# Kernel tuning notes

Hardware: AMD Instinct MI355X
Metric: run time of the kernel (lower is better)

The kernel has to match this reference:

```python
import jax, jax.numpy as jnp
import numpy as np

H = 4      # num_heads
D = 256    # hidden_dim
HD = 64    # head_dim
SCALE = HD ** -0.5


def setup_inputs() -> dict:
    key = jax.random.key(0)
    ks = jax.random.split(key, 5)
    x = jax.random.normal(ks[0], (4, 4096, D), dtype=jnp.float32)
    # Linear weights stored torch-style as [out, in]; y = x @ W.T
    init = 1.0 / np.sqrt(D)
    Wq = jax.random.uniform(ks[1], (D, D), jnp.float32, -init, init)
    Wk = jax.random.uniform(ks[2], (D, D), jnp.float32, -init, init)
    Wv = jax.random.uniform(ks[3], (D, D), jnp.float32, -init, init)
    Wo = jax.random.uniform(ks[4], (D, D), jnp.float32, -init, init)
    return {"x": x, "Wq": Wq, "Wk": Wk, "Wv": Wv, "Wo": Wo}


def reference(x, Wq, Wk, Wv, Wo):
    B, S, _ = x.shape
    # projections (torch Linear: x @ W.T)
    q = (x @ Wq.T).reshape(B, S, H, HD).transpose(0, 2, 1, 3)  # [B,H,S,HD]
    k = (x @ Wk.T).reshape(B, S, H, HD).transpose(0, 2, 1, 3)
    v = (x @ Wv.T).reshape(B, S, H, HD).transpose(0, 2, 1, 3)
    scores = jnp.einsum('bhqd,bhkd->bhqk', q, k) * SCALE  # [B,H,S,S]
    causal = jnp.triu(jnp.ones((S, S), dtype=bool), k=1)
    scores = jnp.where(causal[None, None], -jnp.inf, scores)
    attn = jax.nn.softmax(scores, axis=-1)
    out = jnp.einsum('bhqk,bhkd->bhqd', attn, v)  # [B,H,S,HD]
    out = out.transpose(0, 2, 1, 3).reshape(B, S, D)
    return out @ Wo.T
```

## Files before the change

kernel.cpp:

```cpp
#include <hip/hip_runtime.h>
#include <hip/hip_bf16.h>
#include <cstdint>

using short8  = __attribute__((ext_vector_type(8))) short;
using u16x8   = __attribute__((ext_vector_type(8))) unsigned short;
using u16x4   = __attribute__((ext_vector_type(4))) unsigned short;
using f32x4   = __attribute__((ext_vector_type(4))) float;
using f32x16  = __attribute__((ext_vector_type(16))) float;

constexpr int BN = 4, HN = 4, SN = 4096, DN = 256, HD = 64;
constexpr int MROWS = BN * SN;
constexpr float QSCL = 0.18033688011112042f;

__device__ __forceinline__ unsigned short f2bf(float x) {
  union { float f; unsigned int u; } c; c.f = x;
  unsigned int u = c.u;
  return (unsigned short)((u + 0x7fffu + ((u >> 16) & 1u)) >> 16);
}
__device__ __forceinline__ unsigned int cvt_pk_bf16(float a, float b) {
  unsigned int r;
  asm("v_cvt_pk_bf16_f32 %0, %1, %2" : "=v"(r) : "v"(a), "v"(b));
  return r;
}
__device__ __forceinline__ void pl32swap(unsigned int& a, unsigned int& b) {
  asm volatile("v_permlane32_swap_b32 %0, %1" : "+v"(a), "+v"(b));
}

#define GLDS16(g, l)                                                  \
  __builtin_amdgcn_global_load_lds(                                   \
      (const __attribute__((address_space(1))) void*)(g),             \
      (__attribute__((address_space(3))) void*)(l), 16, 0, 0)

__global__ __launch_bounds__(256) void convert_kernel(
    const float* __restrict__ x,  const float* __restrict__ Wq,
    const float* __restrict__ Wk, const float* __restrict__ Wv,
    const float* __restrict__ Wo,
    unsigned short* __restrict__ xb, unsigned short* __restrict__ Wcat,
    unsigned short* __restrict__ Wob) {
  const long NX4 = (long)MROWS * DN / 4;
  const long NW4 = 65536 / 4;
  const long total = NX4 + 4 * NW4;
  for (long i = (long)blockIdx.x * 256 + threadIdx.x; i < total;
       i += (long)gridDim.x * 256) {
    const float* src; unsigned short* dst;
    if (i < NX4) { src = x + i * 4; dst = xb + i * 4; }
    else {
      long j = i - NX4; int w = (int)(j >> 14); long o = (j & 16383) * 4;
      src = (w == 0 ? Wq : w == 1 ? Wk : w == 2 ? Wv : Wo) + o;
      dst = (w < 3 ? Wcat + (long)w * 65536 : Wob) + o;
    }
    float4 v = *(const float4*)src;
    u16x4 pk; pk[0] = f2bf(v.x); pk[1] = f2bf(v.y);
    pk[2] = f2bf(v.z); pk[3] = f2bf(v.w);
    *(u16x4*)dst = pk;
  }
}

template <int MODE, int NBN>
__global__ __launch_bounds__(256) void gemm_kernel(
    const unsigned short* __restrict__ Abf,
    const unsigned short* __restrict__ Bbf,
    unsigned short* __restrict__ qo, unsigned short* __restrict__ ko,
    unsigned short* __restrict__ vo, float* __restrict__ out) {
  constexpr int SMEM = (MODE == 1) ? 128 * 132 * 4 : 128 * 136 * 2;
  __shared__ __align__(16) char smem[SMEM];
  unsigned short* stg = (unsigned short*)smem;

  const int tid = threadIdx.x, lane = tid & 63, wid = tid >> 6;
  const int lo = lane & 15, hi = lane >> 4;
  const int bn = blockIdx.x % NBN, bm = blockIdx.x / NBN;
  const int wm = (wid >> 1) * 64, wn = (wid & 1) * 64;
  const long arow0 = (long)bm * 128, brow0 = (long)bn * 128;

  auto stage = [&](int buf, int kt) {
    const int row = (wid * 2) * 16 + (lane >> 2);
    const int col = (lane & 3) * 8;
    const unsigned short* ga = Abf + (arow0 + row) * DN + kt * 32 + col;
    const unsigned short* gb = Bbf + (brow0 + row) * DN + kt * 32 + col;
    unsigned short* la = stg + buf * 8192 + wid * 1024;
    unsigned short* lb = la + 4096;
    GLDS16(ga, la);
    GLDS16(ga + 16 * DN, la + 512);
    GLDS16(gb, lb);
    GLDS16(gb + 16 * DN, lb + 512);
  };

  f32x4 acc[4][4];
#pragma unroll
  for (int a = 0; a < 4; ++a)
#pragma unroll
    for (int b = 0; b < 4; ++b)
#pragma unroll
      for (int e = 0; e < 4; ++e) acc[a][b][e] = 0.f;

  stage(0, 0);
#pragma unroll
  for (int kt = 0; kt < 8; ++kt) {
    const int buf = kt & 1;
    __syncthreads();
    if (kt < 7) stage(buf ^ 1, kt + 1);
    const unsigned short* sa = stg + buf * 8192;
    const unsigned short* sb = sa + 4096;
    short8 af[4], bf[4];
#pragma unroll
    for (int f = 0; f < 4; ++f) {
      af[f] = *(const short8*)(sa + (wm + f * 16 + lo) * 32 + hi * 8);
      bf[f] = *(const short8*)(sb + (wn + f * 16 + lo) * 32 + hi * 8);
    }
#pragma unroll
    for (int fn = 0; fn < 4; ++fn)
#pragma unroll
      for (int fm = 0; fm < 4; ++fm)
        acc[fn][fm] = __builtin_amdgcn_mfma_f32_16x16x32_bf16(
            bf[fn], af[fm], acc[fn][fm], 0, 0, 0);
  }
  __syncthreads();

  if constexpr (MODE == 0) {
    unsigned short* cs = (unsigned short*)smem;
    if (bn < 4) {
      const float cscl = (bn < 2) ? QSCL : 1.0f;
#pragma unroll
      for (int fn = 0; fn < 4; ++fn)
#pragma unroll
        for (int fm = 0; fm < 4; ++fm) {
          u16x4 pk;
#pragma unroll
          for (int r = 0; r < 4; ++r) pk[r] = f2bf(acc[fn][fm][r] * cscl);
          const int m = wm + fm * 16 + lo, n0 = wn + fn * 16 + hi * 4;
          *(u16x4*)(cs + m * 136 + n0) = pk;
        }
      __syncthreads();
      unsigned short* dstmat = (bn < 2) ? qo : ko;
      const int colbase = (bn & 1) * 128;
#pragma unroll
      for (int p = 0; p < 8; ++p) {
        const int ml = p * 16 + (tid >> 4), n0 = (tid & 15) * 8;
        u16x8 v = *(u16x8*)(cs + ml * 136 + n0);
        const int c = colbase + n0, h = c >> 6, hd = c & 63;
        const long m = arow0 + ml;
        const int b = (int)(m >> 12), s = (int)(m & 4095);
        *(u16x8*)(dstmat + ((long)(b * HN + h) * SN + s) * HD + hd) = v;
      }
    } else {
#pragma unroll
      for (int fn = 0; fn < 4; ++fn)
#pragma unroll
        for (int fm = 0; fm < 4; ++fm) {
          const int m = wm + fm * 16 + lo, n0 = wn + fn * 16 + hi * 4;
#pragma unroll
          for (int r = 0; r < 4; ++r)
            cs[(n0 + r) * 136 + m] = f2bf(acc[fn][fm][r]);
        }
      __syncthreads();
      const int b = (int)(arow0 >> 12), sbase = (int)(arow0 & 4095);
#pragma unroll
      for (int p = 0; p < 8; ++p) {
        const int cl = p * 16 + (tid >> 4);
        const int s0 = (tid & 15) * 8;
        u16x8 v = *(u16x8*)(cs + cl * 136 + s0);
        const int c = (bn & 1) * 128 + cl, h = c >> 6, hd = c & 63;
        *(u16x8*)(vo + ((long)((b * HN + h) * HD + hd)) * SN + sbase + s0) = v;
      }
    }
  } else {
    float* csf = (float*)smem;
#pragma unroll
    for (int fn = 0; fn < 4; ++fn)
#pragma unroll
      for (int fm = 0; fm < 4; ++fm) {
        const int m = wm + fm * 16 + lo, n0 = wn + fn * 16 + hi * 4;
        *(f32x4*)(csf + m * 132 + n0) = acc[fn][fm];
      }
    __syncthreads();
#pragma unroll
    for (int p = 0; p < 8; ++p) {
      const int ml = p * 16 + (tid >> 4), n0 = (tid & 15) * 8;
      f32x4 v0 = *(f32x4*)(csf + ml * 132 + n0);
      f32x4 v1 = *(f32x4*)(csf + ml * 132 + n0 + 4);
      float* dst = out + (arow0 + ml) * DN + bn * 128 + n0;
      *(f32x4*)dst = v0;
      *(f32x4*)(dst + 4) = v1;
    }
  }
}

template <int NSPLIT>
__global__ __launch_bounds__(256, 2) void attn_kernel(
    const unsigned short* __restrict__ Qw, const unsigned short* __restrict__ Kw,
    const unsigned short* __restrict__ VTp, unsigned short* __restrict__ Ow,
    float* __restrict__ Op, float* __restrict__ Mp, float* __restrict__ Lp) {
  __shared__ __align__(16) unsigned short sK[2][4096];
  __shared__ __align__(16) unsigned short sV[2][4096];

  const int tid = threadIdx.x;
  const int w = tid >> 6, lane = tid & 63;
  const int l31 = lane & 31, h5 = lane >> 5;
  const int bid = blockIdx.x;
  const int bh = (bid & 7) * 2 + ((bid >> 3) & 1);
  int c, g;
  if constexpr (NSPLIT == 2) { c = (bid >> 4) & 1; g = bid >> 5; }
  else { c = 0; g = bid >> 4; }
  const int t = 31 - g;
  const int q0 = t * 128;
  const int qw = q0 + w * 32;
  const long base = (long)bh * SN * HD;
  const int tlast = 2 * t + 1;
  const int wlast = 2 * t + (w >> 1);

  const int sr = w * 16 + (lane >> 3);
  const int gcol8 = (((lane & 7) ^ (lane >> 3)) << 3);
  auto stage = [&](int buf, int k0) {
    const unsigned short* gk = Kw + base + (long)(k0 + sr) * HD + gcol8;
    GLDS16(gk, &sK[buf][w * 1024]);
    GLDS16(gk + 8 * HD, &sK[buf][w * 1024 + 512]);
    const unsigned short* gv = VTp + base + (long)sr * SN + k0 + gcol8;
    GLDS16(gv, &sV[buf][w * 1024]);
    GLDS16(gv + 8 * SN, &sV[buf][w * 1024 + 512]);
  };

  short8 qf[4];
#pragma unroll
  for (int ks = 0; ks < 4; ++ks)
    qf[ks] = *(const short8*)(Qw + base + (long)(qw + l31) * HD + ks * 16 + h5 * 8);

  f32x16 oacc[2];
#pragma unroll
  for (int oh = 0; oh < 2; ++oh)
#pragma unroll
    for (int r = 0; r < 16; ++r) oacc[oh][r] = 0.f;
  float m_ = -INFINITY, l_ = 0.f;

  const int swz = (l31 & 7) << 3;

  stage(0, c * 64);
  __syncthreads();
  int buf = 0;
  for (int kt = c; kt <= tlast; kt += NSPLIT) {
    if (kt + NSPLIT <= tlast) stage(buf ^ 1, (kt + NSPLIT) * 64);

    if (kt <= wlast) {
      const int k0 = kt * 64;
      short8 kb[8];
#pragma unroll
      for (int s = 0; s < 2; ++s)
#pragma unroll
        for (int ks = 0; ks < 4; ++ks)
          kb[s * 4 + ks] = *(const short8*)&sK[buf][(32 * s + l31) * 64 +
                                                   (((2 * ks + h5) << 3) ^ swz)];
      f32x16 c0, c1;
#pragma unroll
      for (int r = 0; r < 16; ++r) { c0[r] = 0.f; c1[r] = 0.f; }
#pragma unroll
      for (int ks = 0; ks < 4; ++ks)
        c0 = __builtin_amdgcn_mfma_f32_32x32x16_bf16(kb[ks], qf[ks], c0, 0, 0, 0);
#pragma unroll
      for (int ks = 0; ks < 4; ++ks)
        c1 = __builtin_amdgcn_mfma_f32_32x32x16_bf16(kb[4 + ks], qf[ks], c1, 0, 0, 0);

      short8 vt0[4], vt1[4];
#pragma unroll
      for (int ks = 0; ks < 4; ++ks) {
        const int col = ((2 * ks + h5) << 3) ^ swz;
        vt0[ks] = *(const short8*)&sV[buf][l31 * 64 + col];
        vt1[ks] = *(const short8*)&sV[buf][(32 + l31) * 64 + col];
      }

      if (kt == wlast) {
        const int mb0 = k0 + 4 * h5 - qw - l31;
#pragma unroll
        for (int r = 0; r < 16; ++r) {
          const int d = (r & 3) + 8 * (r >> 2);
          if (mb0 + d > 0)      c0[r] = -INFINITY;
          if (mb0 + 32 + d > 0) c1[r] = -INFINITY;
        }
      }

      float mv[16];
#pragma unroll
      for (int r = 0; r < 16; ++r) mv[r] = fmaxf(c0[r], c1[r]);
#pragma unroll
      for (int st = 8; st >= 1; st >>= 1)
#pragma unroll
        for (int i = 0; i < st; ++i) mv[i] = fmaxf(mv[i], mv[i + st]);
      const float mx = fmaxf(mv[0], __shfl_xor(mv[0], 32, 64));

      if (__any(mx > m_ + 11.5f)) {
        const float mn = fmaxf(m_, mx);
        const float alpha = __builtin_amdgcn_exp2f(m_ - mn);
        m_ = mn;
        l_ *= alpha;
#pragma unroll
        for (int oh = 0; oh < 2; ++oh)
#pragma unroll
          for (int r = 0; r < 16; ++r) oacc[oh][r] *= alpha;
      }

#pragma unroll
      for (int r = 0; r < 16; ++r) {
        c0[r] = __builtin_amdgcn_exp2f(c0[r] - m_);
        c1[r] = __builtin_amdgcn_exp2f(c1[r] - m_);
      }
      float sv[16];
#pragma unroll
      for (int r = 0; r < 16; ++r) sv[r] = c0[r] + c1[r];
#pragma unroll
      for (int st = 8; st >= 1; st >>= 1)
#pragma unroll
        for (int i = 0; i < st; ++i) sv[i] += sv[i + st];
      l_ += sv[0] + __shfl_xor(sv[0], 32, 64);

      short8 pb[4];
#pragma unroll
      for (int s = 0; s < 2; ++s)
#pragma unroll
        for (int u = 0; u < 2; ++u) {
          unsigned int a0, a1, b0, b1;
          if (s == 0) {
            a0 = cvt_pk_bf16(c0[8 * u + 0], c0[8 * u + 1]);
            a1 = cvt_pk_bf16(c0[8 * u + 2], c0[8 * u + 3]);
            b0 = cvt_pk_bf16(c0[8 * u + 4], c0[8 * u + 5]);
            b1 = cvt_pk_bf16(c0[8 * u + 6], c0[8 * u + 7]);
          } else {
            a0 = cvt_pk_bf16(c1[8 * u + 0], c1[8 * u + 1]);
            a1 = cvt_pk_bf16(c1[8 * u + 2], c1[8 * u + 3]);
            b0 = cvt_pk_bf16(c1[8 * u + 4], c1[8 * u + 5]);
            b1 = cvt_pk_bf16(c1[8 * u + 6], c1[8 * u + 7]);
          }
          pl32swap(a0, b0);
          pl32swap(a1, b1);
          union { unsigned int u4[4]; short8 v; } pu;
          pu.u4[0] = a0; pu.u4[1] = a1; pu.u4[2] = b0; pu.u4[3] = b1;
          pb[s * 2 + u] = pu.v;
        }

#pragma unroll
      for (int ks = 0; ks < 4; ++ks) {
        oacc[0] = __builtin_amdgcn_mfma_f32_32x32x16_bf16(vt0[ks], pb[ks], oacc[0], 0, 0, 0);
        oacc[1] = __builtin_amdgcn_mfma_f32_32x32x16_bf16(vt1[ks], pb[ks], oacc[1], 0, 0, 0);
      }
    }

    __syncthreads();
    buf ^= 1;
  }

  if constexpr (NSPLIT == 1) {
    unsigned short* ob = (unsigned short*)sK;
    const float rl = 1.f / l_;
#pragma unroll
    for (int oh = 0; oh < 2; ++oh)
#pragma unroll
      for (int rq = 0; rq < 4; ++rq) {
        const int hdb = 32 * oh + 8 * rq + 4 * h5;
        const unsigned int u0 = cvt_pk_bf16(oacc[oh][4 * rq + 0] * rl,
                                            oacc[oh][4 * rq + 1] * rl);
        const unsigned int u1 = cvt_pk_bf16(oacc[oh][4 * rq + 2] * rl,
                                            oacc[oh][4 * rq + 3] * rl);
        *(uint2*)&ob[w * 2048 + l31 * 64 + (hdb ^ ((l31 & 7) << 3))] =
            make_uint2(u0, u1);
      }
    __syncthreads();
    const int b = bh >> 2, h = bh & 3;
#pragma unroll
    for (int pass = 0; pass < 4; ++pass) {
      const int idx = pass * 256 + tid;
      const int row = idx >> 3, j = idx & 7;
      const int wreg = row >> 5, qi = row & 31;
      u16x8 vv = *(u16x8*)&ob[wreg * 2048 + qi * 64 +
                              ((j * 8) ^ ((qi & 7) << 3))];
      *(u16x8*)(Ow + ((long)(b * SN + q0 + row)) * DN + h * HD + j * 8) = vv;
    }
  } else {
    const long pb0 = (long)(c * 16 + bh) * 64;
#pragma unroll
    for (int oh = 0; oh < 2; ++oh)
#pragma unroll
      for (int rq = 0; rq < 4; ++rq)
#pragma unroll
        for (int e = 0; e < 4; ++e) {
          const int hd = 32 * oh + 8 * rq + 4 * h5 + e;
          Op[(pb0 + hd) * SN + qw + l31] = oacc[oh][4 * rq + e];
        }
    if (h5 == 0) {
      Mp[(long)(c * 16 + bh) * SN + qw + l31] = m_;
      Lp[(long)(c * 16 + bh) * SN + qw + l31] = l_;
    }
  }
}

__global__ __launch_bounds__(256) void merge_kernel(
    const float* __restrict__ Op, const float* __restrict__ Mp,
    const float* __restrict__ Lp, unsigned short* __restrict__ Ow) {
  __shared__ float w0s[64], w1s[64];
  __shared__ __align__(16) unsigned short obuf[64][72];
  const int tid = threadIdx.x;
  const int bh = blockIdx.x >> 6;
  const int qb = (blockIdx.x & 63) * 64;
  if (tid < 64) {
    const int q = qb + tid;
    const float m0 = Mp[(long)bh * SN + q], m1 = Mp[(long)(16 + bh) * SN + q];
    const float l0 = Lp[(long)bh * SN + q], l1 = Lp[(long)(16 + bh) * SN + q];
    const float ms = fmaxf(m0, m1);
    const float a0 = __builtin_amdgcn_exp2f(m0 - ms);
    const float a1 = __builtin_amdgcn_exp2f(m1 - ms);
    const float rl = 1.f / (l0 * a0 + l1 * a1);
    w0s[tid] = a0 * rl;
    w1s[tid] = a1 * rl;
  }
  __syncthreads();
#pragma unroll
  for (int pass = 0; pass < 16; ++pass) {
    const int idx = pass * 256 + tid;
    const int hd = idx >> 6, q = idx & 63;
    const float v0 = Op[((long)bh * 64 + hd) * SN + qb + q];
    const float v1 = Op[((long)(16 + bh) * 64 + hd) * SN + qb + q];
    obuf[q][hd ^ ((q & 7) << 3)] = f2bf(v0 * w0s[q] + v1 * w1s[q]);
  }
  __syncthreads();
  const int b = bh >> 2, h = bh & 3;
#pragma unroll
  for (int pass = 0; pass < 4; ++pass) {
    const int idx = pass * 256 + tid;
    const int q = idx >> 4, hg = (idx & 15) * 4;
    uint2 v = *(uint2*)&obuf[q][hg ^ ((q & 7) << 3)];
    *(uint2*)(Ow + ((long)(b * SN + qb + q)) * DN + h * HD + hg) = v;
  }
}

extern "C" void kernel_launch(void* const* d_in, const int* in_sizes, int n_in,
                              void* d_out, int out_size, void* d_ws, size_t ws_size,
                              hipStream_t stream) {
  const float* x  = (const float*)d_in[0];
  const float* Wq = (const float*)d_in[1];
  const float* Wk = (const float*)d_in[2];
  const float* Wv = (const float*)d_in[3];
  const float* Wo = (const float*)d_in[4];
  float* out = (float*)d_out;

  const size_t per = (size_t)MROWS * DN;
  unsigned short* xb   = (unsigned short*)d_ws;
  unsigned short* Wcat = xb + per;
  unsigned short* Wob  = Wcat + 768 * 256;
  unsigned short* Qw   = Wob + 65536;
  unsigned short* Kw   = Qw + per;
  unsigned short* VTw  = Kw + per;
  unsigned short* Ow   = xb;
  const size_t base_bytes = (4 * per + 768 * 256 + 65536) * sizeof(unsigned short);
  float* Op = (float*)((char*)d_ws + base_bytes);
  float* Mp = Op + (size_t)2 * 16 * 64 * SN;
  float* Lp = Mp + (size_t)2 * 16 * SN;
  const size_t need = base_bytes +
      ((size_t)2 * 16 * 64 * SN + 2 * (size_t)2 * 16 * SN) * sizeof(float);

  convert_kernel<<<2048, 256, 0, stream>>>(x, Wq, Wk, Wv, Wo, xb, Wcat, Wob);
  gemm_kernel<0, 6><<<6 * (MROWS / 128), 256, 0, stream>>>(
      xb, Wcat, Qw, Kw, VTw, nullptr);
  if (ws_size >= need) {
    attn_kernel<2><<<1024, 256, 0, stream>>>(Qw, Kw, VTw, nullptr, Op, Mp, Lp);
    merge_kernel<<<16 * (SN / 64), 256, 0, stream>>>(Op, Mp, Lp, Ow);
  } else {
    attn_kernel<1><<<512, 256, 0, stream>>>(
        Qw, Kw, VTw, Ow, nullptr, nullptr, nullptr);
  }
  gemm_kernel<1, 2><<<2 * (MROWS / 128), 256, 0, stream>>>(
      Ow, Wob, nullptr, nullptr, nullptr, out);
}
```

Measured before the change: 93.17 us.

## Pair causal query tiles per block for balanced work and add MFMA priority

Each attention block now processes two query tiles, t and 31-t, so every block does roughly equal causal work, and the grid is halved. MFMA sections are wrapped in s_setprio to favor matrix issue, and the row-max reduction is rewritten as a flatter max tree. This targets tail imbalance from the causal triangle but reduces the number of blocks in flight and serializes two tiles per block, including an extra stage and sync per phase.

```diff
diff --git a/kernel.cpp b/kernel.cpp
--- a/kernel.cpp
+++ b/kernel.cpp
@@ -198,15 +198,9 @@
   const int l31 = lane & 31, h5 = lane >> 5;
   const int bid = blockIdx.x;
   const int bh = (bid & 7) * 2 + ((bid >> 3) & 1);
-  int c, g;
-  if constexpr (NSPLIT == 2) { c = (bid >> 4) & 1; g = bid >> 5; }
-  else { c = 0; g = bid >> 4; }
-  const int t = 31 - g;
-  const int q0 = t * 128;
-  const int qw = q0 + w * 32;
+  const int pair = (bid >> 4) & 15;
+  const int c = (NSPLIT == 2) ? ((bid >> 8) & 1) : 0;
   const long base = (long)bh * SN * HD;
-  const int tlast = 2 * t + 1;
-  const int wlast = 2 * t + (w >> 1);
 
   const int sr = w * 16 + (lane >> 3);
   const int gcol8 = (((lane & 7) ^ (lane >> 3)) << 3);
@@ -219,172 +213,191 @@
     GLDS16(gv + 8 * SN, &sV[buf][w * 1024 + 512]);
   };
 
-  short8 qf[4];
-#pragma unroll
-  for (int ks = 0; ks < 4; ++ks)
-    qf[ks] = *(const short8*)(Qw + base + (long)(qw + l31) * HD + ks * 16 + h5 * 8);
-
-  f32x16 oacc[2];
-#pragma unroll
-  for (int oh = 0; oh < 2; ++oh)
-#pragma unroll
-    for (int r = 0; r < 16; ++r) oacc[oh][r] = 0.f;
-  float m_ = -INFINITY, l_ = 0.f;
-
   const int swz = (l31 & 7) << 3;
 
-  stage(0, c * 64);
-  __syncthreads();
-  int buf = 0;
-  for (int kt = c; kt <= tlast; kt += NSPLIT) {
-    if (kt + NSPLIT <= tlast) stage(buf ^ 1, (kt + NSPLIT) * 64);
-
-    if (kt <= wlast) {
-      const int k0 = kt * 64;
-      short8 kb[8];
-#pragma unroll
-      for (int s = 0; s < 2; ++s)
+#pragma unroll
+  for (int ph = 0; ph < 2; ++ph) {
+    const int t = ph ? (31 - pair) : pair;
+    const int q0 = t * 128;
+    const int qw = q0 + w * 32;
+    const int tlast = 2 * t + 1;
+    const int wlast = 2 * t + (w >> 1);
+
+    short8 qf[4];
+#pragma unroll
+    for (int ks = 0; ks < 4; ++ks)
+      qf[ks] = *(const short8*)(Qw + base + (long)(qw + l31) * HD +
+                                ks * 16 + h5 * 8);
+
+    f32x16 oacc[2];
+#pragma unroll
+    for (int oh = 0; oh < 2; ++oh)
+#pragma unroll
+      for (int r = 0; r < 16; ++r) oacc[oh][r] = 0.f;
+    float m_ = -INFINITY, l_ = 0.f;
+
+    stage(0, c * 64);
+    __syncthreads();
+    int buf = 0;
+    for (int kt = c; kt <= tlast; kt += NSPLIT) {
+      if (kt + NSPLIT <= tlast) stage(buf ^ 1, (kt + NSPLIT) * 64);
+
+      if (kt <= wlast) {
+        const int k0 = kt * 64;
+        short8 kb[8];
+#pragma unroll
+        for (int s = 0; s < 2; ++s)
+#pragma unroll
+          for (int ks = 0; ks < 4; ++ks)
+            kb[s * 4 + ks] = *(const short8*)&sK[buf][(32 * s + l31) * 64 +
+                                                 (((2 * ks + h5) << 3) ^ swz)];
+        f32x16 c0, c1;
+#pragma unroll
+        for (int r = 0; r < 16; ++r) { c0[r] = 0.f; c1[r] = 0.f; }
+        __builtin_amdgcn_s_setprio(1);
 #pragma unroll
         for (int ks = 0; ks < 4; ++ks)
-          kb[s * 4 + ks] = *(const short8*)&sK[buf][(32 * s + l31) * 64 +
-                                                   (((2 * ks + h5) << 3) ^ swz)];
-      f32x16 c0, c1;
-#pragma unroll
-      for (int r = 0; r < 16; ++r) { c0[r] = 0.f; c1[r] = 0.f; }
-#pragma unroll
-      for (int ks = 0; ks < 4; ++ks)
-        c0 = __builtin_amdgcn_mfma_f32_32x32x16_bf16(kb[ks], qf[ks], c0, 0, 0, 0);
-#pragma unroll
-      for (int ks = 0; ks < 4; ++ks)
-        c1 = __builtin_amdgcn_mfma_f32_32x32x16_bf16(kb[4 + ks], qf[ks], c1, 0, 0, 0);
-
-      short8 vt0[4], vt1[4];
-#pragma unroll
-      for (int ks = 0; ks < 4; ++ks) {
-        const int col = ((2 * ks + h5) << 3) ^ swz;
-        vt0[ks] = *(const short8*)&sV[buf][l31 * 64 + col];
-        vt1[ks] = *(const short8*)&sV[buf][(32 + l31) * 64 + col];
-      }
-
-      if (kt == wlast) {
-        const int mb0 = k0 + 4 * h5 - qw - l31;
+          c0 = __builtin_amdgcn_mfma_f32_32x32x16_bf16(kb[ks], qf[ks], c0, 0, 0, 0);
+#pragma unroll
+        for (int ks = 0; ks < 4; ++ks)
+          c1 = __builtin_amdgcn_mfma_f32_32x32x16_bf16(kb[4 + ks], qf[ks], c1, 0, 0, 0);
+        __builtin_amdgcn_s_setprio(0);
+
+        short8 vt0[4], vt1[4];
+#pragma unroll
+        for (int ks = 0; ks < 4; ++ks) {
+          const int col = ((2 * ks + h5) << 3) ^ swz;
+          vt0[ks] = *(const short8*)&sV[buf][l31 * 64 + col];
+          vt1[ks] = *(const short8*)&sV[buf][(32 + l31) * 64 + col];
+        }
+
+        if (kt == wlast) {
+          const int mb0 = k0 + 4 * h5 - qw - l31;
+#pragma unroll
+          for (int r = 0; r < 16; ++r) {
+            const int d = (r & 3) + 8 * (r >> 2);
+            if (mb0 + d > 0)      c0[r] = -INFINITY;
+            if (mb0 + 32 + d > 0) c1[r] = -INFINITY;
+          }
+        }
+
+        float mv[16];
+#pragma unroll
+        for (int r = 0; r < 16; ++r) mv[r] = fmaxf(c0[r], c1[r]);
+        const float t0 = fmaxf(fmaxf(mv[0], mv[1]), mv[2]);
+        const float t1 = fmaxf(fmaxf(mv[3], mv[4]), mv[5]);
+        const float t2 = fmaxf(fmaxf(mv[6], mv[7]), mv[8]);
+        const float t3 = fmaxf(fmaxf(mv[9], mv[10]), mv[11]);
+        const float t4 = fmaxf(fmaxf(mv[12], mv[13]), mv[14]);
+        const float t5 = fmaxf(fmaxf(t0, t1), t2);
+        const float t6 = fmaxf(fmaxf(t3, t4), mv[15]);
+        const float mxl = fmaxf(t5, t6);
+        const float mx = fmaxf(mxl, __shfl_xor(mxl, 32, 64));
+
+        if (__any(mx > m_ + 11.5f)) {
+          const float mn = fmaxf(m_, mx);
+          const float alpha = __builtin_amdgcn_exp2f(m_ - mn);
+          m_ = mn;
+          l_ *= alpha;
+#pragma unroll
+          for (int oh = 0; oh < 2; ++oh)
+#pragma unroll
+            for (int r = 0; r < 16; ++r) oacc[oh][r] *= alpha;
+        }
+
 #pragma unroll
         for (int r = 0; r < 16; ++r) {
-          const int d = (r & 3) + 8 * (r >> 2);
-          if (mb0 + d > 0)      c0[r] = -INFINITY;
-          if (mb0 + 32 + d > 0) c1[r] = -INFINITY;
-        }
-      }
-
-      float mv[16];
-#pragma unroll
-      for (int r = 0; r < 16; ++r) mv[r] = fmaxf(c0[r], c1[r]);
-#pragma unroll
-      for (int st = 8; st >= 1; st >>= 1)
-#pragma unroll
-        for (int i = 0; i < st; ++i) mv[i] = fmaxf(mv[i], mv[i + st]);
-      const float mx = fmaxf(mv[0], __shfl_xor(mv[0], 32, 64));
-
-      if (__any(mx > m_ + 11.5f)) {
-        const float mn = fmaxf(m_, mx);
-        const float alpha = __builtin_amdgcn_exp2f(m_ - mn);
-        m_ = mn;
-        l_ *= alpha;
-#pragma unroll
-        for (int oh = 0; oh < 2; ++oh)
-#pragma unroll
-          for (int r = 0; r < 16; ++r) oacc[oh][r] *= alpha;
-      }
-
-#pragma unroll
-      for (int r = 0; r < 16; ++r) {
-        c0[r] = __builtin_amdgcn_exp2f(c0[r] - m_);
-        c1[r] = __builtin_amdgcn_exp2f(c1[r] - m_);
-      }
-      float sv[16];
-#pragma unroll
-      for (int r = 0; r < 16; ++r) sv[r] = c0[r] + c1[r];
-#pragma unroll
-      for (int st = 8; st >= 1; st >>= 1)
-#pragma unroll
-        for (int i = 0; i < st; ++i) sv[i] += sv[i + st];
-      l_ += sv[0] + __shfl_xor(sv[0], 32, 64);
-
-      short8 pb[4];
-#pragma unroll
-      for (int s = 0; s < 2; ++s)
-#pragma unroll
-        for (int u = 0; u < 2; ++u) {
-          unsigned int a0, a1, b0, b1;
-          if (s == 0) {
-            a0 = cvt_pk_bf16(c0[8 * u + 0], c0[8 * u + 1]);
-            a1 = cvt_pk_bf16(c0[8 * u + 2], c0[8 * u + 3]);
-            b0 = cvt_pk_bf16(c0[8 * u + 4], c0[8 * u + 5]);
-            b1 = cvt_pk_bf16(c0[8 * u + 6], c0[8 * u + 7]);
-          } else {
-            a0 = cvt_pk_bf16(c1[8 * u + 0], c1[8 * u + 1]);
-            a1 = cvt_pk_bf16(c1[8 * u + 2], c1[8 * u + 3]);
-            b0 = cvt_pk_bf16(c1[8 * u + 4], c1[8 * u + 5]);
-            b1 = cvt_pk_bf16(c1[8 * u + 6], c1[8 * u + 7]);
+          c0[r] = __builtin_amdgcn_exp2f(c0[r] - m_);
+          c1[r] = __builtin_amdgcn_exp2f(c1[r] - m_);
+        }
+        float sv[16];
+#pragma unroll
+        for (int r = 0; r < 16; ++r) sv[r] = c0[r] + c1[r];
+#pragma unroll
+        for (int st = 8; st >= 1; st >>= 1)
+#pragma unroll
+          for (int i = 0; i < st; ++i) sv[i] += sv[i + st];
+        l_ += sv[0] + __shfl_xor(sv[0], 32, 64);
+
+        short8 pb[4];
+#pragma unroll
+        for (int s = 0; s < 2; ++s)
+#pragma unroll
+          for (int u = 0; u < 2; ++u) {
+            unsigned int a0, a1, b0, b1;
+            if (s == 0) {
+              a0 = cvt_pk_bf16(c0[8 * u + 0], c0[8 * u + 1]);
+              a1 = cvt_pk_bf16(c0[8 * u + 2], c0[8 * u + 3]);
+              b0 = cvt_pk_bf16(c0[8 * u + 4], c0[8 * u + 5]);
+              b1 = cvt_pk_bf16(c0[8 * u + 6], c0[8 * u + 7]);
+            } else {
+              a0 = cvt_pk_bf16(c1[8 * u + 0], c1[8 * u + 1]);
+              a1 = cvt_pk_bf16(c1[8 * u + 2], c1[8 * u + 3]);
+              b0 = cvt_pk_bf16(c1[8 * u + 4], c1[8 * u + 5]);
+              b1 = cvt_pk_bf16(c1[8 * u + 6], c1[8 * u + 7]);
+            }
+            pl32swap(a0, b0);
+            pl32swap(a1, b1);
+            union { unsigned int u4[4]; short8 v; } pu;
+            pu.u4[0] = a0; pu.u4[1] = a1; pu.u4[2] = b0; pu.u4[3] = b1;
+            pb[s * 2 + u] = pu.v;
           }
-          pl32swap(a0, b0);
-          pl32swap(a1, b1);
-          union { unsigned int u4[4]; short8 v; } pu;
-          pu.u4[0] = a0; pu.u4[1] = a1; pu.u4[2] = b0; pu.u4[3] = b1;
-          pb[s * 2 + u] = pu.v;
-        }
-
-#pragma unroll
-      for (int ks = 0; ks < 4; ++ks) {
-        oacc[0] = __builtin_amdgcn_mfma_f32_32x32x16_bf16(vt0[ks], pb[ks], oacc[0], 0, 0, 0);
-        oacc[1] = __builtin_amdgcn_mfma_f32_32x32x16_bf16(vt1[ks], pb[ks], oacc[1], 0, 0, 0);
-      }
-    }
-
-    __syncthreads();
-    buf ^= 1;
-  }
-
-  if constexpr (NSPLIT == 1) {
-    unsigned short* ob = (unsigned short*)sK;
-    const float rl = 1.f / l_;
-#pragma unroll
-    for (int oh = 0; oh < 2; ++oh)
-#pragma unroll
-      for (int rq = 0; rq < 4; ++rq) {
-        const int hdb = 32 * oh + 8 * rq + 4 * h5;
-        const unsigned int u0 = cvt_pk_bf16(oacc[oh][4 * rq + 0] * rl,
-                                            oacc[oh][4 * rq + 1] * rl);
-        const unsigned int u1 = cvt_pk_bf16(oacc[oh][4 * rq + 2] * rl,
-                                            oacc[oh][4 * rq + 3] * rl);
-        *(uint2*)&ob[w * 2048 + l31 * 64 + (hdb ^ ((l31 & 7) << 3))] =
-            make_uint2(u0, u1);
-      }
-    __syncthreads();
-    const int b = bh >> 2, h = bh & 3;
-#pragma unroll
-    for (int pass = 0; pass < 4; ++pass) {
-      const int idx = pass * 256 + tid;
-      const int row = idx >> 3, j = idx & 7;
-      const int wreg = row >> 5, qi = row & 31;
-      u16x8 vv = *(u16x8*)&ob[wreg * 2048 + qi * 64 +
-                              ((j * 8) ^ ((qi & 7) << 3))];
-      *(u16x8*)(Ow + ((long)(b * SN + q0 + row)) * DN + h * HD + j * 8) = vv;
-    }
-  } else {
-    const long pb0 = (long)(c * 16 + bh) * 64;
-#pragma unroll
-    for (int oh = 0; oh < 2; ++oh)
-#pragma unroll
-      for (int rq = 0; rq < 4; ++rq)
-#pragma unroll
-        for (int e = 0; e < 4; ++e) {
-          const int hd = 32 * oh + 8 * rq + 4 * h5 + e;
-          Op[(pb0 + hd) * SN + qw + l31] = oacc[oh][4 * rq + e];
-        }
-    if (h5 == 0) {
-      Mp[(long)(c * 16 + bh) * SN + qw + l31] = m_;
-      Lp[(long)(c * 16 + bh) * SN + qw + l31] = l_;
+
+        __builtin_amdgcn_s_setprio(1);
+#pragma unroll
+        for (int ks = 0; ks < 4; ++ks) {
+          oacc[0] = __builtin_amdgcn_mfma_f32_32x32x16_bf16(vt0[ks], pb[ks], oacc[0], 0, 0, 0);
+          oacc[1] = __builtin_amdgcn_mfma_f32_32x32x16_bf16(vt1[ks], pb[ks], oacc[1], 0, 0, 0);
+        }
+        __builtin_amdgcn_s_setprio(0);
+      }
+
+      __syncthreads();
+      buf ^= 1;
+    }
+
+    if constexpr (NSPLIT == 1) {
+      unsigned short* ob = (unsigned short*)sK;
+      const float rl = 1.f / l_;
+#pragma unroll
+      for (int oh = 0; oh < 2; ++oh)
+#pragma unroll
+        for (int rq = 0; rq < 4; ++rq) {
+          const int hdb = 32 * oh + 8 * rq + 4 * h5;
+          const unsigned int u0 = cvt_pk_bf16(oacc[oh][4 * rq + 0] * rl,
+                                              oacc[oh][4 * rq + 1] * rl);
+          const unsigned int u1 = cvt_pk_bf16(oacc[oh][4 * rq + 2] * rl,
+                                              oacc[oh][4 * rq + 3] * rl);
+          *(uint2*)&ob[w * 2048 + l31 * 64 + (hdb ^ ((l31 & 7) << 3))] =
+              make_uint2(u0, u1);
+        }
+      __syncthreads();
+      const int b = bh >> 2, h = bh & 3;
+#pragma unroll
+      for (int pass = 0; pass < 4; ++pass) {
+        const int idx = pass * 256 + tid;
+        const int row = idx >> 3, j = idx & 7;
+        const int wreg = row >> 5, qi = row & 31;
+        u16x8 vv = *(u16x8*)&ob[wreg * 2048 + qi * 64 +
+                                ((j * 8) ^ ((qi & 7) << 3))];
+        *(u16x8*)(Ow + ((long)(b * SN + q0 + row)) * DN + h * HD + j * 8) = vv;
+      }
+      __syncthreads();
+    } else {
+      const long pb0 = (long)(c * 16 + bh) * 64;
+#pragma unroll
+      for (int oh = 0; oh < 2; ++oh)
+#pragma unroll
+        for (int rq = 0; rq < 4; ++rq)
+#pragma unroll
+          for (int e = 0; e < 4; ++e) {
+            const int hd = 32 * oh + 8 * rq + 4 * h5 + e;
+            Op[(pb0 + hd) * SN + qw + l31] = oacc[oh][4 * rq + e];
+          }
+      if (h5 == 0) {
+        Mp[(long)(c * 16 + bh) * SN + qw + l31] = m_;
+        Lp[(long)(c * 16 + bh) * SN + qw + l31] = l_;
+      }
     }
   }
 }
@@ -457,10 +470,10 @@
   gemm_kernel<0, 6><<<6 * (MROWS / 128), 256, 0, stream>>>(
       xb, Wcat, Qw, Kw, VTw, nullptr);
   if (ws_size >= need) {
-    attn_kernel<2><<<1024, 256, 0, stream>>>(Qw, Kw, VTw, nullptr, Op, Mp, Lp);
+    attn_kernel<2><<<512, 256, 0, stream>>>(Qw, Kw, VTw, nullptr, Op, Mp, Lp);
     merge_kernel<<<16 * (SN / 64), 256, 0, stream>>>(Op, Mp, Lp, Ow);
   } else {
-    attn_kernel<1><<<512, 256, 0, stream>>>(
+    attn_kernel<1><<<256, 256, 0, stream>>>(
         Qw, Kw, VTw, Ow, nullptr, nullptr, nullptr);
   }
   gemm_kernel<1, 2><<<2 * (MROWS / 128), 256, 0, stream>>>(
```

New measurement: 102.4 us. 1.1x slower.
